# Optimization experiments

Hardware: AMD Instinct MI355X
Metric: run time of the kernel (lower is better)

The kernel has to match this reference:

```python
import jax, jax.numpy as jnp
import numpy as np

# NF4 codebook (bitsandbytes nf4 data type, 16 levels)
NF4_TABLE = np.array([
    -1.0, -0.6961928009986877, -0.5250730514526367, -0.39491748809814453,
    -0.28444138169288635, -0.18477343022823334, -0.09105003625154495, 0.0,
    0.07958029955625534, 0.16093020141124725, 0.24611230194568634,
    0.33791524171829224, 0.44070982933044434, 0.5626170039176941,
    0.7229568362236023, 1.0], dtype=np.float32)

BLOCKSIZE = 64
SCALING = 32.0 / 16.0  # lora_alpha / r


def setup_inputs() -> dict:
    key = jax.random.key(0)
    k1, k2, k3, k4, k5 = jax.random.split(key, 5)
    tokens, in_f, out_f, r = 256, 4096, 11008, 16
    x = jax.random.normal(k1, (tokens, in_f), dtype=jnp.float32)
    q_codes = jax.random.randint(k2, (out_f, in_f), 0, 16, dtype=jnp.int32)
    absmax = jax.random.uniform(k3, (out_f, in_f // BLOCKSIZE), dtype=jnp.float32)
    lora_A = jax.random.normal(k4, (r, in_f), dtype=jnp.float32) * (1.0 / np.sqrt(in_f))
    lora_B = jax.random.normal(k5, (out_f, r), dtype=jnp.float32) * 0.02
    return {"x": x, "q_codes": q_codes, "absmax": absmax,
            "lora_A": lora_A, "lora_B": lora_B}


def reference(x, q_codes, absmax, lora_A, lora_B):
    out_f, in_f = q_codes.shape
    nf4 = jnp.asarray(NF4_TABLE, dtype=x.dtype)
    # Dequantize: codebook lookup, then per-block absmax scale.
    W = nf4[q_codes].reshape(out_f, in_f // BLOCKSIZE, BLOCKSIZE)
    W = (W * absmax[:, :, None]).reshape(out_f, in_f)  # [out_f, in_f]
    # Base 4-bit linear (no bias in bnb Linear4bit default here).
    base = x @ W.T  # [tokens, out_f]
    # LoRA path: dropout p=0 is identity in eval; scaling = alpha/r.
    lora = (x @ lora_A.T) @ lora_B.T  # [tokens, r] -> [tokens, out_f]
    return base + lora * jnp.asarray(SCALING, dtype=x.dtype)
```

## Files before the change

### kernel.cpp

```cpp
#include <hip/hip_runtime.h>
#include <hip/hip_fp16.h>

typedef unsigned int uint;
typedef unsigned short ushort;

typedef __attribute__((ext_vector_type(8))) _Float16 f16x8;
typedef __attribute__((ext_vector_type(4))) float f32x4;

#define TOK 256
#define OUTF 11008
#define INF 4096
#define BM 256
#define BN 64
#define NT2 172

__device__ __constant__ float NF4_TBL[16] = {
    -1.0f, -0.6961928009986877f, -0.5250730514526367f, -0.39491748809814453f,
    -0.28444138169288635f, -0.18477343022823334f, -0.09105003625154495f, 0.0f,
    0.07958029955625534f, 0.16093020141124725f, 0.24611230194568634f,
    0.33791524171829224f, 0.44070982933044434f, 0.5626170039176941f,
    0.7229568362236023f, 1.0f};

__device__ __forceinline__ ushort f2h(float f) {
  return __half_as_ushort(__float2half(f));
}

__device__ __forceinline__ void async_cp16(const void* g, void* l) {
  __builtin_amdgcn_global_load_lds(
      (const __attribute__((address_space(1))) uint*)g,
      (__attribute__((address_space(3))) uint*)l, 16, 0, 0);
}

__device__ __forceinline__ float nf4v(int c, int tbits) {
  return __int_as_float(__builtin_amdgcn_ds_bpermute(c << 2, tbits));
}

__device__ __forceinline__ uint2 dq4(int4 c, __half2 ax2, int tbits) {
  __half2 h0 = __floats2half2_rn(nf4v(c.x, tbits), nf4v(c.y, tbits));
  __half2 h1 = __floats2half2_rn(nf4v(c.z, tbits), nf4v(c.w, tbits));
  h0 = __hmul2(h0, ax2);
  h1 = __hmul2(h1, ax2);
  union { __half2 h[2]; uint2 u; } r;
  r.h[0] = h0; r.h[1] = h1;
  return r.u;
}

__device__ __forceinline__ void step_barrier() {
  asm volatile("s_waitcnt lgkmcnt(0)" ::: "memory");
  __builtin_amdgcn_s_barrier();
}

__global__ void prep_kernel(const float* __restrict__ x, uint4* __restrict__ xf4,
                            const float4* __restrict__ lB4, ushort4* __restrict__ lBh4) {
  const int stride = gridDim.x * blockDim.x;
  const int t0 = blockIdx.x * blockDim.x + threadIdx.x;
  for (int f = t0; f < TOK * INF / 8; f += stride) {
    int l = f & 63;
    int rlo = l & 15, chunk = l >> 4;
    int ms = (f >> 6) & 7;
    int mt = ms >> 1, ks2 = ms & 1;
    int w = (f >> 9) & 3;
    int kb = f >> 11;
    int m = w * 64 + mt * 16 + rlo;
    int k0 = kb * 64 + (ks2 * 4 + chunk) * 8;
    const float4* src = (const float4*)(x + (size_t)m * INF + k0);
    float4 v0 = src[0], v1 = src[1];
    union { ushort4 h[2]; uint4 u; } pk;
    pk.h[0].x = f2h(v0.x); pk.h[0].y = f2h(v0.y); pk.h[0].z = f2h(v0.z); pk.h[0].w = f2h(v0.w);
    pk.h[1].x = f2h(v1.x); pk.h[1].y = f2h(v1.y); pk.h[1].z = f2h(v1.z); pk.h[1].w = f2h(v1.w);
    xf4[f] = pk.u;
  }
  for (int i = t0; i < OUTF * 16; i += stride) {
    int n = i >> 4, jq = i & 15;
    ushort4 o = {0, 0, 0, 0};
    if (jq < 4) {
      float4 v = lB4[n * 4 + jq];
      o.x = f2h(v.x); o.y = f2h(v.y); o.z = f2h(v.z); o.w = f2h(v.w);
    }
    lBh4[i] = o;
  }
}

__global__ __launch_bounds__(1024)
void xa_kernel(const float* __restrict__ x, const float* __restrict__ lA,
               ushort* __restrict__ xa2) {
  const int m = blockIdx.x;
  const int t = threadIdx.x;
  const float4* x4 = (const float4*)(x + (size_t)m * INF);
  const float4* lA4 = (const float4*)lA;
  float4 xv = x4[t];
  float acc[16];
#pragma unroll
  for (int j = 0; j < 16; ++j) {
    float4 a = lA4[j * (INF / 4) + t];
    acc[j] = xv.x * a.x + xv.y * a.y + xv.z * a.z + xv.w * a.w;
  }
#pragma unroll
  for (int j = 0; j < 16; ++j)
#pragma unroll
    for (int s = 32; s > 0; s >>= 1) acc[j] += __shfl_xor(acc[j], s, 64);
  __shared__ float red[16][16];
  const int w = t >> 6, l = t & 63;
  if (l == 0) {
#pragma unroll
    for (int j = 0; j < 16; ++j) red[w][j] = acc[j];
  }
  __syncthreads();
  if (t < 64) {
    ushort v = 0;
    if (t < 16) {
      float s = 0.f;
#pragma unroll
      for (int w2 = 0; w2 < 16; ++w2) s += red[w2][t];
      v = f2h(2.0f * s);
    }
    xa2[m * 64 + t] = v;
  }
}

__global__ __launch_bounds__(256, 2)
void gemm_kernel(const int* __restrict__ qc, const float* __restrict__ am,
                 const ushort* __restrict__ xf, const ushort* __restrict__ lBh,
                 const ushort* __restrict__ xa2, float* __restrict__ dest, int nst) {
  __shared__ ushort Bbuf[2][64 * 64];
  __shared__ float Qax[4096];

  const int tid = threadIdx.x;
  const int w = tid >> 6;
  const int l = tid & 63;
  const int chunk = l >> 4;
  const int rlo = l & 15;
  const int split = blockIdx.x / NT2;
  const int ntile = blockIdx.x - split * NT2;
  const int n0 = ntile * BN;
  const int kb0 = split * nst;

  const int tbits = __float_as_int(NF4_TBL[l & 15]);

  const int qrg = tid >> 4;
  const int qch = tid & 15;
  const int* qbase[4];
  int bdst[4];
#pragma unroll
  for (int p = 0; p < 4; ++p) {
    int r = p * 16 + qrg;
    qbase[p] = qc + (size_t)(n0 + r) * INF + kb0 * 64 + qch * 4;
    bdst[p] = r * 64 + (((qch >> 1) ^ (r & 7)) << 3) + (qch & 1) * 4;
  }

  int boff[2][4];
#pragma unroll
  for (int ks2 = 0; ks2 < 2; ++ks2)
#pragma unroll
    for (int nt = 0; nt < 4; ++nt)
      boff[ks2][nt] = (nt * 16 + rlo) * 64 + (((ks2 * 4 + chunk) ^ (rlo & 7)) << 3);

  f32x4 acc[4][4];
#pragma unroll
  for (int mt = 0; mt < 4; ++mt)
#pragma unroll
    for (int nt = 0; nt < 4; ++nt) acc[mt][nt] = (f32x4){0.f, 0.f, 0.f, 0.f};

  auto loadA = [&](f16x8 ar[2][4], int kb) {
    const ushort* base = xf + ((size_t)kb * 4 + w) * 4096 + (size_t)l * 8;
#pragma unroll
    for (int mt = 0; mt < 4; ++mt)
#pragma unroll
      for (int ks2 = 0; ks2 < 2; ++ks2)
        ar[ks2][mt] = *(const f16x8*)(base + (mt * 2 + ks2) * 512);
  };

  auto loadQ = [&](int4 q[4], int s) {
#pragma unroll
    for (int p = 0; p < 4; ++p) q[p] = *(const int4*)(qbase[p] + (size_t)s * 64);
  };

  auto dequantF = [&](int4 q[4], int kbt, ushort* bb) {
#pragma unroll
    for (int p = 0; p < 4; ++p) {
      int r = p * 16 + qrg;
      __half2 ax2 = __float2half2_rn(Qax[(kbt >> 2) * 256 + r * 4 + (kbt & 3)]);
      *(uint2*)&bb[bdst[p]] = dq4(q[p], ax2, tbits);
    }
  };

  auto compute = [&](f16x8 ar[2][4], const ushort* bb) {
    __builtin_amdgcn_s_setprio(1);
#pragma unroll
    for (int ks2 = 0; ks2 < 2; ++ks2) {
      f16x8 b[4];
#pragma unroll
      for (int nt = 0; nt < 4; ++nt) b[nt] = *(const f16x8*)&bb[boff[ks2][nt]];
#pragma unroll
      for (int mt = 0; mt < 4; ++mt)
#pragma unroll
        for (int nt = 0; nt < 4; ++nt)
          acc[mt][nt] = __builtin_amdgcn_mfma_f32_16x16x32_f16(ar[ks2][mt], b[nt], acc[mt][nt], 0, 0, 0);
    }
    __builtin_amdgcn_s_setprio(0);
  };

  if (w == 0) {
#pragma unroll
    for (int j = 0; j < 16; ++j)
      async_cp16(am + (size_t)(n0 + l) * 64 + j * 4, (char*)Qax + j * 1024);
  }
  f16x8 arA[2][4], arB[2][4];
  int4 qA[4], qB[4];
  loadA(arA, kb0);
  loadA(arB, kb0 + 1);
  loadQ(qA, 0);
  loadQ(qB, 1);
  __syncthreads();
  dequantF(qA, kb0, Bbuf[0]);
  step_barrier();

  for (int s = 0; s < nst; s += 2) {
    compute(arA, Bbuf[0]);
    if (s + 1 < nst) dequantF(qB, kb0 + s + 1, Bbuf[1]);
    if (s + 2 < nst) {
      loadA(arA, kb0 + s + 2);
      loadQ(qA, s + 2);
    }
    step_barrier();
    compute(arB, Bbuf[1]);
    if (s + 2 < nst) dequantF(qA, kb0 + s + 2, Bbuf[0]);
    if (s + 3 < nst) {
      loadA(arB, kb0 + s + 3);
      loadQ(qB, s + 3);
    }
    step_barrier();
  }

  if (split == 0) {
    f16x8 a_l[4], b_l[4];
#pragma unroll
    for (int mt = 0; mt < 4; ++mt)
      a_l[mt] = *(const f16x8*)(xa2 + (size_t)(w * 64 + mt * 16 + rlo) * 64 + chunk * 8);
#pragma unroll
    for (int nt = 0; nt < 4; ++nt)
      b_l[nt] = *(const f16x8*)(lBh + (size_t)(n0 + nt * 16 + rlo) * 64 + chunk * 8);
#pragma unroll
    for (int mt = 0; mt < 4; ++mt)
#pragma unroll
      for (int nt = 0; nt < 4; ++nt)
        acc[mt][nt] = __builtin_amdgcn_mfma_f32_16x16x32_f16(a_l[mt], b_l[nt], acc[mt][nt], 0, 0, 0);
  }

  float* dst = dest + (size_t)split * TOK * OUTF;
#pragma unroll
  for (int mt = 0; mt < 4; ++mt) {
#pragma unroll
    for (int nt = 0; nt < 4; ++nt) {
      int c = n0 + nt * 16 + rlo;
#pragma unroll
      for (int r = 0; r < 4; ++r) {
        int row = w * 64 + mt * 16 + chunk * 4 + r;
        dst[(size_t)row * OUTF + c] = acc[mt][nt][r];
      }
    }
  }
}

__global__ void reduce_kernel(const float4* __restrict__ part, float4* __restrict__ out,
                              int ks) {
  const int QN = TOK * OUTF / 4;
  int i = blockIdx.x * blockDim.x + threadIdx.x;
  if (i < QN) {
    float4 s = part[i];
    for (int s2 = 1; s2 < ks; ++s2) {
      float4 p = part[(size_t)s2 * QN + i];
      s.x += p.x; s.y += p.y; s.z += p.z; s.w += p.w;
    }
    out[i] = s;
  }
}

extern "C" void kernel_launch(void* const* d_in, const int* in_sizes, int n_in,
                              void* d_out, int out_size, void* d_ws, size_t ws_size,
                              hipStream_t stream) {
  const float* x = (const float*)d_in[0];
  const int* qc = (const int*)d_in[1];
  const float* am = (const float*)d_in[2];
  const float* lA = (const float*)d_in[3];
  const float* lB = (const float*)d_in[4];
  float* out = (float*)d_out;

  const size_t off_lB = (size_t)TOK * INF * 2;
  const size_t off_xa2 = off_lB + (size_t)OUTF * 64 * 2;
  const size_t off_part = off_xa2 + (size_t)TOK * 64 * 2;
  const size_t part_bytes = (size_t)TOK * OUTF * 4;

  ushort* xf = (ushort*)d_ws;
  ushort* lBh = (ushort*)((char*)d_ws + off_lB);
  ushort* xa2 = (ushort*)((char*)d_ws + off_xa2);
  float* part = (float*)((char*)d_ws + off_part);

  int ks = 1;
  if (ws_size >= off_part + 4 * part_bytes) ks = 4;
  else if (ws_size >= off_part + 2 * part_bytes) ks = 2;
  float* dest = (ks == 1) ? out : part;

  prep_kernel<<<2048, 256, 0, stream>>>(x, (uint4*)xf, (const float4*)lB,
                                        (ushort4*)lBh);
  xa_kernel<<<TOK, 1024, 0, stream>>>(x, lA, xa2);
  gemm_kernel<<<NT2 * ks, 256, 0, stream>>>(qc, am, xf, lBh, xa2, dest, 64 / ks);
  if (ks > 1)
    reduce_kernel<<<(TOK * OUTF / 4 + 255) / 256, 256, 0, stream>>>((const float4*)part,
                                                                    (float4*)out, ks);
}
```

Before: 318.2 us.

## Store split-K partials in fp16, raise split to 8, fuse prep kernels

Partial sums from split-K now go out as fp16 instead of fp32. That halves partial-buffer traffic for both the GEMM stores and the reduce kernel. The split factor goes up to 8 when the workspace allows, and the launch bounds raise occupancy to 4 blocks per CU. The x/lora_B conversion and the x·A LoRA kernels are merged into one launch, and the Q loads are issued earlier in the pipeline loop. Rounding partial sums to fp16 adds precision loss and overflow risk.

```diff
diff --git a/kernel.cpp b/kernel.cpp
--- a/kernel.cpp
+++ b/kernel.cpp
@@ -50,78 +50,79 @@
   __builtin_amdgcn_s_barrier();
 }
 
-__global__ void prep_kernel(const float* __restrict__ x, uint4* __restrict__ xf4,
-                            const float4* __restrict__ lB4, ushort4* __restrict__ lBh4) {
-  const int stride = gridDim.x * blockDim.x;
-  const int t0 = blockIdx.x * blockDim.x + threadIdx.x;
-  for (int f = t0; f < TOK * INF / 8; f += stride) {
-    int l = f & 63;
-    int rlo = l & 15, chunk = l >> 4;
-    int ms = (f >> 6) & 7;
-    int mt = ms >> 1, ks2 = ms & 1;
-    int w = (f >> 9) & 3;
-    int kb = f >> 11;
-    int m = w * 64 + mt * 16 + rlo;
-    int k0 = kb * 64 + (ks2 * 4 + chunk) * 8;
-    const float4* src = (const float4*)(x + (size_t)m * INF + k0);
-    float4 v0 = src[0], v1 = src[1];
-    union { ushort4 h[2]; uint4 u; } pk;
-    pk.h[0].x = f2h(v0.x); pk.h[0].y = f2h(v0.y); pk.h[0].z = f2h(v0.z); pk.h[0].w = f2h(v0.w);
-    pk.h[1].x = f2h(v1.x); pk.h[1].y = f2h(v1.y); pk.h[1].z = f2h(v1.z); pk.h[1].w = f2h(v1.w);
-    xf4[f] = pk.u;
-  }
-  for (int i = t0; i < OUTF * 16; i += stride) {
-    int n = i >> 4, jq = i & 15;
-    ushort4 o = {0, 0, 0, 0};
-    if (jq < 4) {
-      float4 v = lB4[n * 4 + jq];
-      o.x = f2h(v.x); o.y = f2h(v.y); o.z = f2h(v.z); o.w = f2h(v.w);
-    }
-    lBh4[i] = o;
-  }
-}
-
 __global__ __launch_bounds__(1024)
-void xa_kernel(const float* __restrict__ x, const float* __restrict__ lA,
-               ushort* __restrict__ xa2) {
-  const int m = blockIdx.x;
-  const int t = threadIdx.x;
-  const float4* x4 = (const float4*)(x + (size_t)m * INF);
-  const float4* lA4 = (const float4*)lA;
-  float4 xv = x4[t];
-  float acc[16];
-#pragma unroll
-  for (int j = 0; j < 16; ++j) {
-    float4 a = lA4[j * (INF / 4) + t];
-    acc[j] = xv.x * a.x + xv.y * a.y + xv.z * a.z + xv.w * a.w;
-  }
-#pragma unroll
-  for (int j = 0; j < 16; ++j)
-#pragma unroll
-    for (int s = 32; s > 0; s >>= 1) acc[j] += __shfl_xor(acc[j], s, 64);
-  __shared__ float red[16][16];
-  const int w = t >> 6, l = t & 63;
-  if (l == 0) {
-#pragma unroll
-    for (int j = 0; j < 16; ++j) red[w][j] = acc[j];
-  }
-  __syncthreads();
-  if (t < 64) {
-    ushort v = 0;
-    if (t < 16) {
-      float s = 0.f;
-#pragma unroll
-      for (int w2 = 0; w2 < 16; ++w2) s += red[w2][t];
-      v = f2h(2.0f * s);
-    }
-    xa2[m * 64 + t] = v;
-  }
-}
-
-__global__ __launch_bounds__(256, 2)
+void prep_kernel(const float* __restrict__ x, uint4* __restrict__ xf4,
+                 const float4* __restrict__ lB4, ushort4* __restrict__ lBh4,
+                 const float* __restrict__ lA, ushort* __restrict__ xa2) {
+  if (blockIdx.x < 256) {
+    const int stride = 256 * 1024;
+    const int t0 = blockIdx.x * 1024 + threadIdx.x;
+    for (int f = t0; f < TOK * INF / 8; f += stride) {
+      int l = f & 63;
+      int rlo = l & 15, chunk = l >> 4;
+      int ms = (f >> 6) & 7;
+      int mt = ms >> 1, ks2 = ms & 1;
+      int w = (f >> 9) & 3;
+      int kb = f >> 11;
+      int m = w * 64 + mt * 16 + rlo;
+      int k0 = kb * 64 + (ks2 * 4 + chunk) * 8;
+      const float4* src = (const float4*)(x + (size_t)m * INF + k0);
+      float4 v0 = src[0], v1 = src[1];
+      union { ushort4 h[2]; uint4 u; } pk;
+      pk.h[0].x = f2h(v0.x); pk.h[0].y = f2h(v0.y); pk.h[0].z = f2h(v0.z); pk.h[0].w = f2h(v0.w);
+      pk.h[1].x = f2h(v1.x); pk.h[1].y = f2h(v1.y); pk.h[1].z = f2h(v1.z); pk.h[1].w = f2h(v1.w);
+      xf4[f] = pk.u;
+    }
+    for (int i = t0; i < OUTF * 16; i += stride) {
+      int n = i >> 4, jq = i & 15;
+      ushort4 o = {0, 0, 0, 0};
+      if (jq < 4) {
+        float4 v = lB4[n * 4 + jq];
+        o.x = f2h(v.x); o.y = f2h(v.y); o.z = f2h(v.z); o.w = f2h(v.w);
+      }
+      lBh4[i] = o;
+    }
+  } else {
+    const int m = blockIdx.x - 256;
+    const int t = threadIdx.x;
+    const float4* x4 = (const float4*)(x + (size_t)m * INF);
+    const float4* lA4 = (const float4*)lA;
+    float4 xv = x4[t];
+    float acc[16];
+#pragma unroll
+    for (int j = 0; j < 16; ++j) {
+      float4 a = lA4[j * (INF / 4) + t];
+      acc[j] = xv.x * a.x + xv.y * a.y + xv.z * a.z + xv.w * a.w;
+    }
+#pragma unroll
+    for (int j = 0; j < 16; ++j)
+#pragma unroll
+      for (int s = 32; s > 0; s >>= 1) acc[j] += __shfl_xor(acc[j], s, 64);
+    __shared__ float red[16][16];
+    const int w = t >> 6, l = t & 63;
+    if (l == 0) {
+#pragma unroll
+      for (int j = 0; j < 16; ++j) red[w][j] = acc[j];
+    }
+    __syncthreads();
+    if (t < 64) {
+      ushort v = 0;
+      if (t < 16) {
+        float s = 0.f;
+#pragma unroll
+        for (int w2 = 0; w2 < 16; ++w2) s += red[w2][t];
+        v = f2h(2.0f * s);
+      }
+      xa2[m * 64 + t] = v;
+    }
+  }
+}
+
+__global__ __launch_bounds__(256, 4)
 void gemm_kernel(const int* __restrict__ qc, const float* __restrict__ am,
                  const ushort* __restrict__ xf, const ushort* __restrict__ lBh,
-                 const ushort* __restrict__ xa2, float* __restrict__ dest, int nst) {
+                 const ushort* __restrict__ xa2, float* __restrict__ dest32,
+                 ushort* __restrict__ dest16, int nst, int fp16out) {
   __shared__ ushort Bbuf[2][64 * 64];
   __shared__ float Qax[4096];
 
@@ -216,19 +217,15 @@
   step_barrier();
 
   for (int s = 0; s < nst; s += 2) {
+    if (s + 2 < nst) loadQ(qA, s + 2);
     compute(arA, Bbuf[0]);
+    if (s + 2 < nst) loadA(arA, kb0 + s + 2);
     if (s + 1 < nst) dequantF(qB, kb0 + s + 1, Bbuf[1]);
-    if (s + 2 < nst) {
-      loadA(arA, kb0 + s + 2);
-      loadQ(qA, s + 2);
-    }
     step_barrier();
+    if (s + 3 < nst) loadQ(qB, s + 3);
     compute(arB, Bbuf[1]);
+    if (s + 3 < nst) loadA(arB, kb0 + s + 3);
     if (s + 2 < nst) dequantF(qA, kb0 + s + 2, Bbuf[0]);
-    if (s + 3 < nst) {
-      loadA(arB, kb0 + s + 3);
-      loadQ(qB, s + 3);
-    }
     step_barrier();
   }
 
@@ -247,32 +244,54 @@
         acc[mt][nt] = __builtin_amdgcn_mfma_f32_16x16x32_f16(a_l[mt], b_l[nt], acc[mt][nt], 0, 0, 0);
   }
 
-  float* dst = dest + (size_t)split * TOK * OUTF;
-#pragma unroll
-  for (int mt = 0; mt < 4; ++mt) {
-#pragma unroll
-    for (int nt = 0; nt < 4; ++nt) {
-      int c = n0 + nt * 16 + rlo;
-#pragma unroll
-      for (int r = 0; r < 4; ++r) {
-        int row = w * 64 + mt * 16 + chunk * 4 + r;
-        dst[(size_t)row * OUTF + c] = acc[mt][nt][r];
+  if (fp16out) {
+    ushort* dst = dest16 + (size_t)split * TOK * OUTF;
+#pragma unroll
+    for (int mt = 0; mt < 4; ++mt) {
+#pragma unroll
+      for (int nt = 0; nt < 4; ++nt) {
+        int c = n0 + nt * 16 + rlo;
+#pragma unroll
+        for (int r = 0; r < 4; ++r) {
+          int row = w * 64 + mt * 16 + chunk * 4 + r;
+          dst[(size_t)row * OUTF + c] = f2h(acc[mt][nt][r]);
+        }
       }
     }
-  }
-}
-
-__global__ void reduce_kernel(const float4* __restrict__ part, float4* __restrict__ out,
+  } else {
+    float* dst = dest32;
+#pragma unroll
+    for (int mt = 0; mt < 4; ++mt) {
+#pragma unroll
+      for (int nt = 0; nt < 4; ++nt) {
+        int c = n0 + nt * 16 + rlo;
+#pragma unroll
+        for (int r = 0; r < 4; ++r) {
+          int row = w * 64 + mt * 16 + chunk * 4 + r;
+          dst[(size_t)row * OUTF + c] = acc[mt][nt][r];
+        }
+      }
+    }
+  }
+}
+
+__global__ void reduce_kernel(const uint4* __restrict__ part, float4* __restrict__ out,
                               int ks) {
-  const int QN = TOK * OUTF / 4;
+  const int QN8 = TOK * OUTF / 8;
   int i = blockIdx.x * blockDim.x + threadIdx.x;
-  if (i < QN) {
-    float4 s = part[i];
-    for (int s2 = 1; s2 < ks; ++s2) {
-      float4 p = part[(size_t)s2 * QN + i];
-      s.x += p.x; s.y += p.y; s.z += p.z; s.w += p.w;
-    }
-    out[i] = s;
+  if (i < QN8) {
+    float s0 = 0.f, s1 = 0.f, s2 = 0.f, s3 = 0.f, s4 = 0.f, s5 = 0.f, s6 = 0.f, s7 = 0.f;
+    for (int sp = 0; sp < ks; ++sp) {
+      uint4 v = part[(size_t)sp * QN8 + i];
+      union { uint u; __half2 h; } a, b, c, d;
+      a.u = v.x; b.u = v.y; c.u = v.z; d.u = v.w;
+      float2 fa = __half22float2(a.h), fb = __half22float2(b.h);
+      float2 fc = __half22float2(c.h), fd = __half22float2(d.h);
+      s0 += fa.x; s1 += fa.y; s2 += fb.x; s3 += fb.y;
+      s4 += fc.x; s5 += fc.y; s6 += fd.x; s7 += fd.y;
+    }
+    out[2 * i] = (float4){s0, s1, s2, s3};
+    out[2 * i + 1] = (float4){s4, s5, s6, s7};
   }
 }
 
@@ -289,23 +308,24 @@
   const size_t off_lB = (size_t)TOK * INF * 2;
   const size_t off_xa2 = off_lB + (size_t)OUTF * 64 * 2;
   const size_t off_part = off_xa2 + (size_t)TOK * 64 * 2;
-  const size_t part_bytes = (size_t)TOK * OUTF * 4;
+  const size_t part_bytes = (size_t)TOK * OUTF * 2;
 
   ushort* xf = (ushort*)d_ws;
   ushort* lBh = (ushort*)((char*)d_ws + off_lB);
   ushort* xa2 = (ushort*)((char*)d_ws + off_xa2);
-  float* part = (float*)((char*)d_ws + off_part);
+  ushort* part = (ushort*)((char*)d_ws + off_part);
 
   int ks = 1;
-  if (ws_size >= off_part + 4 * part_bytes) ks = 4;
+  if (ws_size >= off_part + 8 * part_bytes) ks = 8;
+  else if (ws_size >= off_part + 4 * part_bytes) ks = 4;
   else if (ws_size >= off_part + 2 * part_bytes) ks = 2;
-  float* dest = (ks == 1) ? out : part;
-
-  prep_kernel<<<2048, 256, 0, stream>>>(x, (uint4*)xf, (const float4*)lB,
-                                        (ushort4*)lBh);
-  xa_kernel<<<TOK, 1024, 0, stream>>>(x, lA, xa2);
-  gemm_kernel<<<NT2 * ks, 256, 0, stream>>>(qc, am, xf, lBh, xa2, dest, 64 / ks);
+  const int fp16out = (ks > 1) ? 1 : 0;
+
+  prep_kernel<<<512, 1024, 0, stream>>>(x, (uint4*)xf, (const float4*)lB,
+                                        (ushort4*)lBh, lA, xa2);
+  gemm_kernel<<<NT2 * ks, 256, 0, stream>>>(qc, am, xf, lBh, xa2, out, part,
+                                            64 / ks, fp16out);
   if (ks > 1)
-    reduce_kernel<<<(TOK * OUTF / 4 + 255) / 256, 256, 0, stream>>>((const float4*)part,
+    reduce_kernel<<<(TOK * OUTF / 8 + 255) / 256, 256, 0, stream>>>((const uint4*)part,
                                                                     (float4*)out, ks);
 }
```

Result: slower. 533.0 us (+67.5%).
